# Performance work log

Hardware: AMD Instinct MI355X
Metric: run time of the kernel (lower is better)

## Reference

```python
import jax, jax.numpy as jnp
import numpy as np

N_EMBED = 8192
EMBED_DIM = 32
BETA = 0.25
EPS_NORM = 1e-12   # torch F.normalize eps
EPS_ENT = 1e-4     # get_entropy eps


def _l2norm(x):
    n = jnp.linalg.norm(x, axis=-1, keepdims=True)
    return x / jnp.maximum(n, EPS_NORM)


def setup_inputs() -> dict:
    key = jax.random.key(0)
    k1, k2 = jax.random.split(key)
    z = jax.random.normal(k1, (32, EMBED_DIM, 32, 32), dtype=jnp.float32)
    # embedding.weight.data.uniform_(-1/n_embed, 1/n_embed)
    embedding = jax.random.uniform(k2, (N_EMBED, EMBED_DIM), dtype=jnp.float32,
                                   minval=-1.0 / N_EMBED, maxval=1.0 / N_EMBED)
    return {"z": z, "embedding": embedding}


def reference(z, embedding):
    batch = z.shape[0]
    # bchw -> bhwc
    zt = jnp.transpose(z, (0, 2, 3, 1))
    # l2_norm branch: cosine distance via negative inner product
    zn = _l2norm(zt)
    z_flat = zn.reshape(-1, EMBED_DIM)            # [N, D], N = B*H*W
    ew = _l2norm(embedding)                       # [K, D]
    d = -jnp.matmul(z_flat, ew.T)                 # [N, K] distance matrix
    idx = jnp.argmin(jax.lax.stop_gradient(d), axis=1)  # [N]
    # codebook usage histogram + entropy
    cb_usage = jax.ops.segment_sum(jnp.ones_like(idx, dtype=jnp.float32), idx,
                                   num_segments=N_EMBED)
    probs = (cb_usage + EPS_ENT) / jnp.sum(cb_usage + EPS_ENT)
    cb_entropy = -jnp.sum(probs * jnp.log(probs))
    # gather + re-normalize (faithful to embedding lookup then F.normalize)
    z_q = _l2norm(embedding[idx]).reshape(zn.shape)
    sg = jax.lax.stop_gradient
    loss = (BETA * jnp.mean(jnp.sum((sg(z_q) - zn) ** 2, axis=-1))
            + jnp.mean(jnp.sum((z_q - sg(zn)) ** 2, axis=-1)))
    # straight-through estimator
    z_q_st = zn + sg(z_q - zn)
    z_q_out = jnp.transpose(z_q_st, (0, 3, 1, 2))  # bhwc -> bchw
    return z_q_out, loss, cb_entropy, idx.reshape(batch, -1)
```

## Files before the change

kernel.cpp:

```cpp
#include <hip/hip_runtime.h>
#include <math.h>

#define N_EMBED 8192
#define DIM 32
#define NQ 32768

#define QPB 256
#define NQG (NQ / QPB)
#define KSPL 8
#define KCHUNK (N_EMBED / KSPL)
#define TILE 128
#define NTILES (KCHUNK / TILE)
#define NPLANE 8
#define LSTRIDE 130

#define LOSS_OFF  1048576
#define ENT_OFF   1048577
#define IDX_OFF   1048578

typedef __attribute__((ext_vector_type(8))) _Float16 half8;
typedef __attribute__((ext_vector_type(4))) float floatx4;

__global__ __launch_bounds__(256) void prep_kernel(const float* __restrict__ e,
                                                   half8* __restrict__ esplit,
                                                   float* __restrict__ inv_norm,
                                                   unsigned* __restrict__ usage,
                                                   float* __restrict__ loss_acc,
                                                   unsigned* __restrict__ done_ctr) {
    int k = blockIdx.x * 256 + threadIdx.x;
    const float4* src = (const float4*)(e + k * DIM);
    float v[DIM];
    float ss = 0.f;
#pragma unroll
    for (int i = 0; i < 8; ++i) {
        float4 t = src[i];
        v[i*4+0] = t.x; v[i*4+1] = t.y; v[i*4+2] = t.z; v[i*4+3] = t.w;
        ss += t.x*t.x + t.y*t.y + t.z*t.z + t.w*t.w;
    }
    float inv = 1.f / fmaxf(sqrtf(ss), 1e-12f);
    inv_norm[k] = inv;
    usage[k] = 0u;
    if (k == 0) { loss_acc[0] = 0.f; done_ctr[0] = 0u; }

#pragma unroll
    for (int part = 0; part < 4; ++part) {
        half8 h8, m8;
#pragma unroll
        for (int j = 0; j < 8; ++j) {
            float xx = v[part * 8 + j] * inv;
            _Float16 h = (_Float16)xx;
            _Float16 m = (_Float16)((xx - (float)h) * 4096.0f);
            h8[j] = h; m8[j] = m;
        }
        esplit[(0 * 4 + part) * N_EMBED + k] = h8;
        esplit[(1 * 4 + part) * N_EMBED + k] = m8;
    }
}

__global__ __launch_bounds__(256, 4) void score_kernel(const float* __restrict__ z,
                                                       const half8* __restrict__ esplit,
                                                       unsigned long long* __restrict__ keys8) {
    __shared__ half8 lds[2][NPLANE * LSTRIDE];

    const int t = threadIdx.x;
    const int lane = t & 63;
    const int w = t >> 6;
    const int quad = lane >> 4;
    const int lc = lane & 15;
    const int qg = blockIdx.x & (NQG - 1);
    const int kc = blockIdx.x >> 7;
    const int kbase = kc * KCHUNK;
    const int qbase = qg * QPB + w * 64;

    half8 ah[4], am[4];
#pragma unroll
    for (int qt = 0; qt < 4; ++qt) {
        int q = qbase + qt * 16 + lc;
        const float* zp = z + (q >> 10) * (DIM * 1024) + (q & 1023);
        float x[8];
        float ss = 0.f;
#pragma unroll
        for (int j = 0; j < 8; ++j) {
            x[j] = zp[(quad * 8 + j) * 1024];
            ss = fmaf(x[j], x[j], ss);
        }
        ss += __shfl_xor(ss, 16, 64);
        ss += __shfl_xor(ss, 32, 64);
        float inv = 1.f / fmaxf(sqrtf(ss), 1e-12f);
#pragma unroll
        for (int j = 0; j < 8; ++j) {
            float xx = x[j] * inv;
            _Float16 h = (_Float16)xx;
            _Float16 m = (_Float16)((xx - (float)h) * 4096.0f);
            ah[qt][j] = h; am[qt][j] = m;
        }
    }

    float best[16];
    int bk[16];
#pragma unroll
    for (int i = 0; i < 16; ++i) { best[i] = -2.0f; bk[i] = 0; }

    const floatx4 z4 = {0.f, 0.f, 0.f, 0.f};

#pragma unroll
    for (int j = 0; j < 4; ++j) {
        int c = t + j * 256; int p = c >> 7, i = c & 127;
        lds[0][p * LSTRIDE + i] = esplit[p * N_EMBED + kbase + i];
    }
    __syncthreads();

    for (int kt = 0; kt < NTILES; ++kt) {
        half8 st[4];
        if (kt + 1 < NTILES) {
#pragma unroll
            for (int j = 0; j < 4; ++j) {
                int c = t + j * 256; int p = c >> 7, i = c & 127;
                st[j] = esplit[p * N_EMBED + kbase + (kt + 1) * TILE + i];
            }
        }
        const half8* __restrict__ buf = lds[kt & 1];
#pragma unroll 2
        for (int ct = 0; ct < TILE / 16; ++ct) {
            half8 bh = buf[(0 * 4 + quad) * LSTRIDE + ct * 16 + lc];
            half8 bm = buf[(1 * 4 + quad) * LSTRIDE + ct * 16 + lc];
            const int kk = kbase + kt * TILE + ct * 16 + lc;
#pragma unroll
            for (int qt = 0; qt < 4; ++qt) {
                floatx4 a0 = __builtin_amdgcn_mfma_f32_16x16x32_f16(ah[qt], bh, z4, 0, 0, 0);
                floatx4 a1 = __builtin_amdgcn_mfma_f32_16x16x32_f16(ah[qt], bm, z4, 0, 0, 0);
                a1 = __builtin_amdgcn_mfma_f32_16x16x32_f16(am[qt], bh, a1, 0, 0, 0);
#pragma unroll
                for (int r = 0; r < 4; ++r) {
                    float d = fmaf(a1[r], 0x1p-12f, a0[r]);
                    if (d > best[qt * 4 + r]) { best[qt * 4 + r] = d; bk[qt * 4 + r] = kk; }
                }
            }
        }
        __syncthreads();
        if (kt + 1 < NTILES) {
#pragma unroll
            for (int j = 0; j < 4; ++j) {
                int c = t + j * 256; int p = c >> 7, i = c & 127;
                lds[(kt + 1) & 1][p * LSTRIDE + i] = st[j];
            }
            __syncthreads();
        }
    }

#pragma unroll
    for (int i = 0; i < 16; ++i) {
        unsigned ub = __float_as_uint(best[i]);
        ub = (ub & 0x80000000u) ? ~ub : (ub | 0x80000000u);
        unsigned long long key = ((unsigned long long)ub << 32) | (unsigned)(~bk[i]);
#pragma unroll
        for (int msk = 1; msk <= 8; msk <<= 1) {
            unsigned long long o = __shfl_xor(key, msk, 64);
            key = (o > key) ? o : key;
        }
        if (lc == 0) {
            int qt = i >> 2, r = i & 3;
            int q = qbase + qt * 16 + quad * 4 + r;
            keys8[kc * NQ + q] = key;
        }
    }
}

__global__ __launch_bounds__(256) void finalize_kernel(const float* __restrict__ z,
                                                       const float* __restrict__ e,
                                                       const float* __restrict__ inv_norm,
                                                       const unsigned long long* __restrict__ keys8,
                                                       unsigned* __restrict__ usage,
                                                       float* __restrict__ loss_acc,
                                                       unsigned* __restrict__ done_ctr,
                                                       float* __restrict__ out) {
    int n = blockIdx.x * 256 + threadIdx.x;
    int b  = n >> 10;
    int hw = n & 1023;
    const float* zb = z + b * (DIM * 1024) + hw;

    float q[DIM];
    float ss = 0.f;
#pragma unroll
    for (int d = 0; d < DIM; ++d) {
        q[d] = zb[d * 1024];
        ss = fmaf(q[d], q[d], ss);
    }
    float inv = 1.f / fmaxf(sqrtf(ss), 1e-12f);
#pragma unroll
    for (int d = 0; d < DIM; ++d) q[d] *= inv;

    float bestd = -1e30f;
    int idx = 0;
#pragma unroll
    for (int c = 0; c < 8; ++c) {
        unsigned long long key = keys8[c * NQ + n];
        int k = (int)(~(unsigned)(key & 0xFFFFFFFFull));
        const float4* er = (const float4*)(e + k * DIM);
        float dot = 0.f;
#pragma unroll
        for (int d8 = 0; d8 < 8; ++d8) {
            float4 t4 = er[d8];
            dot = fmaf(t4.x, q[d8*4+0], dot);
            dot = fmaf(t4.y, q[d8*4+1], dot);
            dot = fmaf(t4.z, q[d8*4+2], dot);
            dot = fmaf(t4.w, q[d8*4+3], dot);
        }
        dot *= inv_norm[k];
        if (dot > bestd) { bestd = dot; idx = k; }
    }

    atomicAdd(&usage[idx], 1u);

    float inv2 = inv_norm[idx];
    const float4* er = (const float4*)(e + idx * DIM);
    float lsum = 0.f;
    float* outb = out + b * (DIM * 1024) + hw;
#pragma unroll
    for (int d8 = 0; d8 < 8; ++d8) {
        float4 t4 = er[d8];
        float w4[4] = {t4.x, t4.y, t4.z, t4.w};
#pragma unroll
        for (int j = 0; j < 4; ++j) {
            int d = d8 * 4 + j;
            float zq = w4[j] * inv2;
            float diff = zq - q[d];
            lsum = fmaf(diff, diff, lsum);
            outb[d * 1024] = q[d] + (zq - q[d]);
        }
    }
    out[IDX_OFF + n] = (float)idx;

#pragma unroll
    for (int off = 32; off > 0; off >>= 1)
        lsum += __shfl_down(lsum, off, 64);
    if ((threadIdx.x & 63) == 0)
        atomicAdd(loss_acc, lsum);

    __shared__ unsigned lastflag;
    __syncthreads();
    if (threadIdx.x == 0) {
        __threadfence();
        unsigned prev = __hip_atomic_fetch_add(done_ctr, 1u, __ATOMIC_ACQ_REL,
                                               __HIP_MEMORY_SCOPE_AGENT);
        lastflag = (prev == gridDim.x - 1) ? 1u : 0u;
    }
    __syncthreads();
    if (lastflag) {
        __shared__ double sm[256];
        int t = threadIdx.x;
        double local = 0.0;
        const float denom = 32768.8192f;
        for (int k = t; k < N_EMBED; k += 256) {
            unsigned c = __hip_atomic_load(&usage[k], __ATOMIC_RELAXED,
                                           __HIP_MEMORY_SCOPE_AGENT);
            float p = ((float)c + 1e-4f) / denom;
            local += (double)(-(p * logf(p)));
        }
        sm[t] = local;
        __syncthreads();
        for (int s = 128; s > 0; s >>= 1) {
            if (t < s) sm[t] += sm[t + s];
            __syncthreads();
        }
        if (t == 0) {
            float la = __hip_atomic_load(loss_acc, __ATOMIC_RELAXED,
                                         __HIP_MEMORY_SCOPE_AGENT);
            out[LOSS_OFF] = (float)(1.25 * (double)la / 32768.0);
            out[ENT_OFF]  = (float)sm[0];
        }
    }
}

extern "C" void kernel_launch(void* const* d_in, const int* in_sizes, int n_in,
                              void* d_out, int out_size, void* d_ws, size_t ws_size,
                              hipStream_t stream) {
    const float* z   = (const float*)d_in[0];
    const float* emb = (const float*)d_in[1];
    float* out = (float*)d_out;

    char* ws = (char*)d_ws;
    half8* esplit            = (half8*)ws;
    unsigned long long* keys8= (unsigned long long*)(ws + (1 << 20));
    float* inv_norm          = (float*)(ws + 3 * (1 << 20));
    unsigned* usage          = (unsigned*)(ws + 3 * (1 << 20) + 32768);
    float* loss_acc          = (float*)(ws + 3 * (1 << 20) + 65536);
    unsigned* done_ctr       = (unsigned*)(ws + 3 * (1 << 20) + 65536 + 4);

    prep_kernel<<<N_EMBED / 256, 256, 0, stream>>>(emb, esplit, inv_norm, usage,
                                                   loss_acc, done_ctr);
    score_kernel<<<NQG * KSPL, 256, 0, stream>>>(z, esplit, keys8);
    finalize_kernel<<<NQ / 256, 256, 0, stream>>>(z, emb, inv_norm, keys8, usage,
                                                  loss_acc, done_ctr, out);
}
```

Baseline: 152.0 us.

## Switch scoring to 32x32x16 MFMA tiles and merge split keys directly in finalize

The score kernel now uses 32x32x16 f16 MFMA instructions over 32 queries per wave instead of 16x16x32 over four 16-query tiles. This halves queries per block and doubles the grid, and occupancy drops from 4 to 3 blocks per SIMD. It is meant to cut LDS reads and MFMA issue overhead per useful product. Finalize now takes the max of the eight packed keys instead of recomputing fp32 dot products for each candidate. That removes gather traffic but relies on the split-fp16 score precision for the final argmin.

```diff
diff --git a/kernel.cpp b/kernel.cpp
--- a/kernel.cpp
+++ b/kernel.cpp
@@ -5,7 +5,7 @@
 #define DIM 32
 #define NQ 32768
 
-#define QPB 256
+#define QPB 128
 #define NQG (NQ / QPB)
 #define KSPL 8
 #define KCHUNK (N_EMBED / KSPL)
@@ -19,7 +19,7 @@
 #define IDX_OFF   1048578
 
 typedef __attribute__((ext_vector_type(8))) _Float16 half8;
-typedef __attribute__((ext_vector_type(4))) float floatx4;
+typedef __attribute__((ext_vector_type(16))) float floatx16;
 
 __global__ __launch_bounds__(256) void prep_kernel(const float* __restrict__ e,
                                                    half8* __restrict__ esplit,
@@ -57,7 +57,7 @@
     }
 }
 
-__global__ __launch_bounds__(256, 4) void score_kernel(const float* __restrict__ z,
+__global__ __launch_bounds__(256, 3) void score_kernel(const float* __restrict__ z,
                                                        const half8* __restrict__ esplit,
                                                        unsigned long long* __restrict__ keys8) {
     __shared__ half8 lds[2][NPLANE * LSTRIDE];
@@ -65,34 +65,36 @@
     const int t = threadIdx.x;
     const int lane = t & 63;
     const int w = t >> 6;
-    const int quad = lane >> 4;
-    const int lc = lane & 15;
+    const int kh = lane >> 5;
+    const int col = lane & 31;
     const int qg = blockIdx.x & (NQG - 1);
-    const int kc = blockIdx.x >> 7;
+    const int kc = blockIdx.x >> 8;
     const int kbase = kc * KCHUNK;
-    const int qbase = qg * QPB + w * 64;
-
-    half8 ah[4], am[4];
-#pragma unroll
-    for (int qt = 0; qt < 4; ++qt) {
-        int q = qbase + qt * 16 + lc;
+    const int qbase = qg * QPB + w * 32;
+
+    half8 ah0, ah1, am0, am1;
+    {
+        int q = qbase + col;
         const float* zp = z + (q >> 10) * (DIM * 1024) + (q & 1023);
-        float x[8];
+        float x[16];
         float ss = 0.f;
 #pragma unroll
         for (int j = 0; j < 8; ++j) {
-            x[j] = zp[(quad * 8 + j) * 1024];
-            ss = fmaf(x[j], x[j], ss);
-        }
-        ss += __shfl_xor(ss, 16, 64);
+            x[j]     = zp[(kh * 8 + j) * 1024];
+            x[8 + j] = zp[(16 + kh * 8 + j) * 1024];
+        }
+#pragma unroll
+        for (int j = 0; j < 16; ++j) ss = fmaf(x[j], x[j], ss);
         ss += __shfl_xor(ss, 32, 64);
         float inv = 1.f / fmaxf(sqrtf(ss), 1e-12f);
 #pragma unroll
         for (int j = 0; j < 8; ++j) {
-            float xx = x[j] * inv;
-            _Float16 h = (_Float16)xx;
-            _Float16 m = (_Float16)((xx - (float)h) * 4096.0f);
-            ah[qt][j] = h; am[qt][j] = m;
+            float x0 = x[j] * inv;
+            _Float16 h0 = (_Float16)x0;
+            ah0[j] = h0; am0[j] = (_Float16)((x0 - (float)h0) * 4096.0f);
+            float x1 = x[8 + j] * inv;
+            _Float16 h1 = (_Float16)x1;
+            ah1[j] = h1; am1[j] = (_Float16)((x1 - (float)h1) * 4096.0f);
         }
     }
 
@@ -101,7 +103,9 @@
 #pragma unroll
     for (int i = 0; i < 16; ++i) { best[i] = -2.0f; bk[i] = 0; }
 
-    const floatx4 z4 = {0.f, 0.f, 0.f, 0.f};
+    floatx16 z16;
+#pragma unroll
+    for (int i = 0; i < 16; ++i) z16[i] = 0.f;
 
 #pragma unroll
     for (int j = 0; j < 4; ++j) {
@@ -120,21 +124,26 @@
             }
         }
         const half8* __restrict__ buf = lds[kt & 1];
-#pragma unroll 2
-        for (int ct = 0; ct < TILE / 16; ++ct) {
-            half8 bh = buf[(0 * 4 + quad) * LSTRIDE + ct * 16 + lc];
-            half8 bm = buf[(1 * 4 + quad) * LSTRIDE + ct * 16 + lc];
-            const int kk = kbase + kt * TILE + ct * 16 + lc;
-#pragma unroll
-            for (int qt = 0; qt < 4; ++qt) {
-                floatx4 a0 = __builtin_amdgcn_mfma_f32_16x16x32_f16(ah[qt], bh, z4, 0, 0, 0);
-                floatx4 a1 = __builtin_amdgcn_mfma_f32_16x16x32_f16(ah[qt], bm, z4, 0, 0, 0);
-                a1 = __builtin_amdgcn_mfma_f32_16x16x32_f16(am[qt], bh, a1, 0, 0, 0);
-#pragma unroll
-                for (int r = 0; r < 4; ++r) {
-                    float d = fmaf(a1[r], 0x1p-12f, a0[r]);
-                    if (d > best[qt * 4 + r]) { best[qt * 4 + r] = d; bk[qt * 4 + r] = kk; }
-                }
+#pragma unroll
+        for (int ct = 0; ct < TILE / 32; ++ct) {
+            const half8* bp = buf + ct * 32 + col;
+            half8 bh0 = bp[(0 + kh) * LSTRIDE];
+            half8 bh1 = bp[(2 + kh) * LSTRIDE];
+            half8 bm0 = bp[(4 + kh) * LSTRIDE];
+            half8 bm1 = bp[(6 + kh) * LSTRIDE];
+
+            floatx16 a0 = __builtin_amdgcn_mfma_f32_32x32x16_f16(ah0, bh0, z16, 0, 0, 0);
+            floatx16 a1 = __builtin_amdgcn_mfma_f32_32x32x16_f16(ah0, bm0, z16, 0, 0, 0);
+            a0 = __builtin_amdgcn_mfma_f32_32x32x16_f16(ah1, bh1, a0, 0, 0, 0);
+            a1 = __builtin_amdgcn_mfma_f32_32x32x16_f16(am0, bh0, a1, 0, 0, 0);
+            a1 = __builtin_amdgcn_mfma_f32_32x32x16_f16(ah1, bm1, a1, 0, 0, 0);
+            a1 = __builtin_amdgcn_mfma_f32_32x32x16_f16(am1, bh1, a1, 0, 0, 0);
+
+            const int kk = kbase + kt * TILE + ct * 32 + col;
+#pragma unroll
+            for (int r = 0; r < 16; ++r) {
+                float d = fmaf(a1[r], 0x1p-12f, a0[r]);
+                if (d > best[r]) { best[r] = d; bk[r] = kk; }
             }
         }
         __syncthreads();
@@ -149,19 +158,18 @@
     }
 
 #pragma unroll
-    for (int i = 0; i < 16; ++i) {
-        unsigned ub = __float_as_uint(best[i]);
+    for (int r = 0; r < 16; ++r) {
+        unsigned ub = __float_as_uint(best[r]);
         ub = (ub & 0x80000000u) ? ~ub : (ub | 0x80000000u);
-        unsigned long long key = ((unsigned long long)ub << 32) | (unsigned)(~bk[i]);
-#pragma unroll
-        for (int msk = 1; msk <= 8; msk <<= 1) {
+        unsigned long long key = ((unsigned long long)ub << 32) | (unsigned)(~bk[r]);
+#pragma unroll
+        for (int msk = 1; msk <= 16; msk <<= 1) {
             unsigned long long o = __shfl_xor(key, msk, 64);
             key = (o > key) ? o : key;
         }
-        if (lc == 0) {
-            int qt = i >> 2, r = i & 3;
-            int q = qbase + qt * 16 + quad * 4 + r;
-            keys8[kc * NQ + q] = key;
+        if (col == 0) {
+            int row = (r & 3) + 8 * (r >> 2) + 4 * kh;
+            keys8[kc * NQ + qbase + row] = key;
         }
     }
 }
@@ -190,25 +198,13 @@
 #pragma unroll
     for (int d = 0; d < DIM; ++d) q[d] *= inv;
 
-    float bestd = -1e30f;
-    int idx = 0;
-#pragma unroll
-    for (int c = 0; c < 8; ++c) {
-        unsigned long long key = keys8[c * NQ + n];
-        int k = (int)(~(unsigned)(key & 0xFFFFFFFFull));
-        const float4* er = (const float4*)(e + k * DIM);
-        float dot = 0.f;
-#pragma unroll
-        for (int d8 = 0; d8 < 8; ++d8) {
-            float4 t4 = er[d8];
-            dot = fmaf(t4.x, q[d8*4+0], dot);
-            dot = fmaf(t4.y, q[d8*4+1], dot);
-            dot = fmaf(t4.z, q[d8*4+2], dot);
-            dot = fmaf(t4.w, q[d8*4+3], dot);
-        }
-        dot *= inv_norm[k];
-        if (dot > bestd) { bestd = dot; idx = k; }
-    }
+    unsigned long long bestkey = 0ull;
+#pragma unroll
+    for (int c = 0; c < KSPL; ++c) {
+        unsigned long long k8 = keys8[c * NQ + n];
+        bestkey = (k8 > bestkey) ? k8 : bestkey;
+    }
+    int idx = (int)(~(unsigned)(bestkey & 0xFFFFFFFFull));
 
     atomicAdd(&usage[idx], 1u);
 
```

New measurement: 154.1 us. About the same (+1.4%).

## Fuse codebook prep into score kernel and drop exact fp32 rescoring

Applied to the files above, without the earlier changes.

Removes the separate prep kernel: each score block now loads raw fp32 codebook rows, normalizes them and splits them into fp16 hi/lo parts directly into LDS. The block size grows to 512 and the codebook is split into 16 chunks. Finalize now picks the winner by a max over the packed score/index keys instead of recomputing exact fp32 dot products for each chunk candidate. This saves a launch and the finalize gather work, but every block now redoes the normalization, and the argmin relies only on the split-fp16 scores, which can change tie-breaking.

```diff
diff --git a/kernel.cpp b/kernel.cpp
--- a/kernel.cpp
+++ b/kernel.cpp
@@ -5,9 +5,9 @@
 #define DIM 32
 #define NQ 32768
 
-#define QPB 256
+#define QPB 512
 #define NQG (NQ / QPB)
-#define KSPL 8
+#define KSPL 16
 #define KCHUNK (N_EMBED / KSPL)
 #define TILE 128
 #define NTILES (KCHUNK / TILE)
@@ -21,54 +21,27 @@
 typedef __attribute__((ext_vector_type(8))) _Float16 half8;
 typedef __attribute__((ext_vector_type(4))) float floatx4;
 
-__global__ __launch_bounds__(256) void prep_kernel(const float* __restrict__ e,
-                                                   half8* __restrict__ esplit,
-                                                   float* __restrict__ inv_norm,
-                                                   unsigned* __restrict__ usage,
-                                                   float* __restrict__ loss_acc,
-                                                   unsigned* __restrict__ done_ctr) {
-    int k = blockIdx.x * 256 + threadIdx.x;
-    const float4* src = (const float4*)(e + k * DIM);
-    float v[DIM];
-    float ss = 0.f;
-#pragma unroll
-    for (int i = 0; i < 8; ++i) {
-        float4 t = src[i];
-        v[i*4+0] = t.x; v[i*4+1] = t.y; v[i*4+2] = t.z; v[i*4+3] = t.w;
-        ss += t.x*t.x + t.y*t.y + t.z*t.z + t.w*t.w;
-    }
-    float inv = 1.f / fmaxf(sqrtf(ss), 1e-12f);
-    inv_norm[k] = inv;
-    usage[k] = 0u;
-    if (k == 0) { loss_acc[0] = 0.f; done_ctr[0] = 0u; }
-
-#pragma unroll
-    for (int part = 0; part < 4; ++part) {
-        half8 h8, m8;
-#pragma unroll
-        for (int j = 0; j < 8; ++j) {
-            float xx = v[part * 8 + j] * inv;
-            _Float16 h = (_Float16)xx;
-            _Float16 m = (_Float16)((xx - (float)h) * 4096.0f);
-            h8[j] = h; m8[j] = m;
-        }
-        esplit[(0 * 4 + part) * N_EMBED + k] = h8;
-        esplit[(1 * 4 + part) * N_EMBED + k] = m8;
-    }
-}
-
-__global__ __launch_bounds__(256, 4) void score_kernel(const float* __restrict__ z,
-                                                       const half8* __restrict__ esplit,
-                                                       unsigned long long* __restrict__ keys8) {
+__global__ __launch_bounds__(512, 4) void score_kernel(const float* __restrict__ z,
+                                                       const float* __restrict__ e,
+                                                       unsigned long long* __restrict__ keys16,
+                                                       unsigned* __restrict__ usage,
+                                                       float* __restrict__ loss_acc,
+                                                       unsigned* __restrict__ done_ctr) {
     __shared__ half8 lds[2][NPLANE * LSTRIDE];
 
     const int t = threadIdx.x;
+
+    if (blockIdx.x == 0) {
+        for (int i = t; i < N_EMBED; i += 512) usage[i] = 0u;
+        if (t == 0) { loss_acc[0] = 0.f; done_ctr[0] = 0u; }
+    }
+
     const int lane = t & 63;
     const int w = t >> 6;
     const int quad = lane >> 4;
     const int lc = lane & 15;
     const int qg = blockIdx.x & (NQG - 1);
-    const int kc = blockIdx.x >> 7;
+    const int kc = blockIdx.x >> 6;
     const int kbase = kc * KCHUNK;
     const int qbase = qg * QPB + w * 64;
 
@@ -96,6 +69,31 @@
         }
     }
 
+    auto stage = [&](int bsel, int kt) {
+        const int ci = t >> 2;
+        const int part = t & 3;
+        const int code = kbase + kt * TILE + ci;
+        const float4* er = (const float4*)(e + code * DIM) + part * 2;
+        float4 v0 = er[0], v1 = er[1];
+        float x[8] = {v0.x, v0.y, v0.z, v0.w, v1.x, v1.y, v1.z, v1.w};
+        float ss = 0.f;
+#pragma unroll
+        for (int j = 0; j < 8; ++j) ss = fmaf(x[j], x[j], ss);
+        ss += __shfl_xor(ss, 1, 64);
+        ss += __shfl_xor(ss, 2, 64);
+        float inv = 1.f / fmaxf(sqrtf(ss), 1e-12f);
+        half8 h8, m8;
+#pragma unroll
+        for (int j = 0; j < 8; ++j) {
+            float xx = x[j] * inv;
+            _Float16 h = (_Float16)xx;
+            _Float16 m = (_Float16)((xx - (float)h) * 4096.0f);
+            h8[j] = h; m8[j] = m;
+        }
+        lds[bsel][part * LSTRIDE + ci] = h8;
+        lds[bsel][(4 + part) * LSTRIDE + ci] = m8;
+    };
+
     float best[16];
     int bk[16];
 #pragma unroll
@@ -103,22 +101,12 @@
 
     const floatx4 z4 = {0.f, 0.f, 0.f, 0.f};
 
-#pragma unroll
-    for (int j = 0; j < 4; ++j) {
-        int c = t + j * 256; int p = c >> 7, i = c & 127;
-        lds[0][p * LSTRIDE + i] = esplit[p * N_EMBED + kbase + i];
-    }
+    stage(0, 0);
     __syncthreads();
 
     for (int kt = 0; kt < NTILES; ++kt) {
-        half8 st[4];
-        if (kt + 1 < NTILES) {
-#pragma unroll
-            for (int j = 0; j < 4; ++j) {
-                int c = t + j * 256; int p = c >> 7, i = c & 127;
-                st[j] = esplit[p * N_EMBED + kbase + (kt + 1) * TILE + i];
-            }
-        }
+        if (kt + 1 < NTILES) stage((kt + 1) & 1, kt + 1);
+
         const half8* __restrict__ buf = lds[kt & 1];
 #pragma unroll 2
         for (int ct = 0; ct < TILE / 16; ++ct) {
@@ -138,14 +126,6 @@
             }
         }
         __syncthreads();
-        if (kt + 1 < NTILES) {
-#pragma unroll
-            for (int j = 0; j < 4; ++j) {
-                int c = t + j * 256; int p = c >> 7, i = c & 127;
-                lds[(kt + 1) & 1][p * LSTRIDE + i] = st[j];
-            }
-            __syncthreads();
-        }
     }
 
 #pragma unroll
@@ -161,15 +141,14 @@
         if (lc == 0) {
             int qt = i >> 2, r = i & 3;
             int q = qbase + qt * 16 + quad * 4 + r;
-            keys8[kc * NQ + q] = key;
+            keys16[kc * NQ + q] = key;
         }
     }
 }
 
 __global__ __launch_bounds__(256) void finalize_kernel(const float* __restrict__ z,
                                                        const float* __restrict__ e,
-                                                       const float* __restrict__ inv_norm,
-                                                       const unsigned long long* __restrict__ keys8,
+                                                       const unsigned long long* __restrict__ keys16,
                                                        unsigned* __restrict__ usage,
                                                        float* __restrict__ loss_acc,
                                                        unsigned* __restrict__ done_ctr,
@@ -190,44 +169,35 @@
 #pragma unroll
     for (int d = 0; d < DIM; ++d) q[d] *= inv;
 
-    float bestd = -1e30f;
-    int idx = 0;
-#pragma unroll
-    for (int c = 0; c < 8; ++c) {
-        unsigned long long key = keys8[c * NQ + n];
-        int k = (int)(~(unsigned)(key & 0xFFFFFFFFull));
-        const float4* er = (const float4*)(e + k * DIM);
-        float dot = 0.f;
-#pragma unroll
-        for (int d8 = 0; d8 < 8; ++d8) {
-            float4 t4 = er[d8];
-            dot = fmaf(t4.x, q[d8*4+0], dot);
-            dot = fmaf(t4.y, q[d8*4+1], dot);
-            dot = fmaf(t4.z, q[d8*4+2], dot);
-            dot = fmaf(t4.w, q[d8*4+3], dot);
-        }
-        dot *= inv_norm[k];
-        if (dot > bestd) { bestd = dot; idx = k; }
-    }
+    unsigned long long bestkey = 0ull;
+#pragma unroll
+    for (int c = 0; c < KSPL; ++c) {
+        unsigned long long k16 = keys16[c * NQ + n];
+        bestkey = (k16 > bestkey) ? k16 : bestkey;
+    }
+    int idx = (int)(~(unsigned)(bestkey & 0xFFFFFFFFull));
 
     atomicAdd(&usage[idx], 1u);
 
-    float inv2 = inv_norm[idx];
+    float wv[DIM];
+    float ss2 = 0.f;
     const float4* er = (const float4*)(e + idx * DIM);
+#pragma unroll
+    for (int d8 = 0; d8 < 8; ++d8) {
+        float4 t4 = er[d8];
+        wv[d8*4+0] = t4.x; wv[d8*4+1] = t4.y; wv[d8*4+2] = t4.z; wv[d8*4+3] = t4.w;
+        ss2 += t4.x*t4.x + t4.y*t4.y + t4.z*t4.z + t4.w*t4.w;
+    }
+    float inv2 = 1.f / fmaxf(sqrtf(ss2), 1e-12f);
+
     float lsum = 0.f;
     float* outb = out + b * (DIM * 1024) + hw;
 #pragma unroll
-    for (int d8 = 0; d8 < 8; ++d8) {
-        float4 t4 = er[d8];
-        float w4[4] = {t4.x, t4.y, t4.z, t4.w};
-#pragma unroll
-        for (int j = 0; j < 4; ++j) {
-            int d = d8 * 4 + j;
-            float zq = w4[j] * inv2;
-            float diff = zq - q[d];
-            lsum = fmaf(diff, diff, lsum);
-            outb[d * 1024] = q[d] + (zq - q[d]);
-        }
+    for (int d = 0; d < DIM; ++d) {
+        float zq = wv[d] * inv2;
+        float diff = zq - q[d];
+        lsum = fmaf(diff, diff, lsum);
+        outb[d * 1024] = q[d] + (zq - q[d]);
     }
     out[IDX_OFF + n] = (float)idx;
 
@@ -280,16 +250,13 @@
     float* out = (float*)d_out;
 
     char* ws = (char*)d_ws;
-    half8* esplit            = (half8*)ws;
-    unsigned long long* keys8= (unsigned long long*)(ws + (1 << 20));
-    float* inv_norm          = (float*)(ws + 3 * (1 << 20));
-    unsigned* usage          = (unsigned*)(ws + 3 * (1 << 20) + 32768);
-    float* loss_acc          = (float*)(ws + 3 * (1 << 20) + 65536);
-    unsigned* done_ctr       = (unsigned*)(ws + 3 * (1 << 20) + 65536 + 4);
-
-    prep_kernel<<<N_EMBED / 256, 256, 0, stream>>>(emb, esplit, inv_norm, usage,
-                                                   loss_acc, done_ctr);
-    score_kernel<<<NQG * KSPL, 256, 0, stream>>>(z, esplit, keys8);
-    finalize_kernel<<<NQ / 256, 256, 0, stream>>>(z, emb, inv_norm, keys8, usage,
+    unsigned long long* keys16 = (unsigned long long*)ws;
+    unsigned* usage            = (unsigned*)(ws + (4 << 20));
+    float* loss_acc            = (float*)(ws + (4 << 20) + 32768);
+    unsigned* done_ctr         = (unsigned*)(ws + (4 << 20) + 32768 + 4);
+
+    score_kernel<<<NQG * KSPL, 512, 0, stream>>>(z, emb, keys16, usage,
+                                                 loss_acc, done_ctr);
+    finalize_kernel<<<NQ / 256, 256, 0, stream>>>(z, emb, keys16, usage,
                                                   loss_acc, done_ctr, out);
 }
```

Result: faster. 144.4 us (-5.0%).

## Fuse finalize into score kernel via per-query-group last-block completion counters

Applied to the files above, without the earlier changes.

Removes the separate finalize kernel: each score block bumps a per-query-group counter, and the last of the K-split blocks for that group reduces the 8 partial keys, gathers the winning code, writes outputs and loss, and a global counter triggers the entropy pass. The exact fp32 re-ranking of the 8 chunk winners is replaced by taking the max of the packed approximate score keys, and the inverse-norm buffer is dropped in favour of recomputing the norm of the chosen row. This saves a launch and the re-rank gathers, but adds atomics, fences and tail work on the last blocks, and may change argmin on near-ties.

```diff
diff --git a/kernel.cpp b/kernel.cpp
--- a/kernel.cpp
+++ b/kernel.cpp
@@ -23,10 +23,10 @@
 
 __global__ __launch_bounds__(256) void prep_kernel(const float* __restrict__ e,
                                                    half8* __restrict__ esplit,
-                                                   float* __restrict__ inv_norm,
                                                    unsigned* __restrict__ usage,
+                                                   unsigned* __restrict__ qg_ctr,
                                                    float* __restrict__ loss_acc,
-                                                   unsigned* __restrict__ done_ctr) {
+                                                   unsigned* __restrict__ fin_ctr) {
     int k = blockIdx.x * 256 + threadIdx.x;
     const float4* src = (const float4*)(e + k * DIM);
     float v[DIM];
@@ -38,9 +38,9 @@
         ss += t.x*t.x + t.y*t.y + t.z*t.z + t.w*t.w;
     }
     float inv = 1.f / fmaxf(sqrtf(ss), 1e-12f);
-    inv_norm[k] = inv;
     usage[k] = 0u;
-    if (k == 0) { loss_acc[0] = 0.f; done_ctr[0] = 0u; }
+    if (k < NQG) qg_ctr[k] = 0u;
+    if (k == 0) { loss_acc[0] = 0.f; fin_ctr[0] = 0u; }
 
 #pragma unroll
     for (int part = 0; part < 4; ++part) {
@@ -58,9 +58,17 @@
 }
 
 __global__ __launch_bounds__(256, 4) void score_kernel(const float* __restrict__ z,
+                                                       const float* __restrict__ e,
                                                        const half8* __restrict__ esplit,
-                                                       unsigned long long* __restrict__ keys8) {
+                                                       unsigned long long* __restrict__ keys8,
+                                                       unsigned* __restrict__ usage,
+                                                       unsigned* __restrict__ qg_ctr,
+                                                       float* __restrict__ loss_acc,
+                                                       unsigned* __restrict__ fin_ctr,
+                                                       float* __restrict__ out) {
     __shared__ half8 lds[2][NPLANE * LSTRIDE];
+    __shared__ double sm[256];
+    __shared__ unsigned qflag, eflag;
 
     const int t = threadIdx.x;
     const int lane = t & 63;
@@ -161,113 +169,106 @@
         if (lc == 0) {
             int qt = i >> 2, r = i & 3;
             int q = qbase + qt * 16 + quad * 4 + r;
-            keys8[kc * NQ + q] = key;
-        }
-    }
-}
-
-__global__ __launch_bounds__(256) void finalize_kernel(const float* __restrict__ z,
-                                                       const float* __restrict__ e,
-                                                       const float* __restrict__ inv_norm,
-                                                       const unsigned long long* __restrict__ keys8,
-                                                       unsigned* __restrict__ usage,
-                                                       float* __restrict__ loss_acc,
-                                                       unsigned* __restrict__ done_ctr,
-                                                       float* __restrict__ out) {
-    int n = blockIdx.x * 256 + threadIdx.x;
-    int b  = n >> 10;
-    int hw = n & 1023;
-    const float* zb = z + b * (DIM * 1024) + hw;
-
-    float q[DIM];
-    float ss = 0.f;
-#pragma unroll
-    for (int d = 0; d < DIM; ++d) {
-        q[d] = zb[d * 1024];
-        ss = fmaf(q[d], q[d], ss);
-    }
-    float inv = 1.f / fmaxf(sqrtf(ss), 1e-12f);
-#pragma unroll
-    for (int d = 0; d < DIM; ++d) q[d] *= inv;
-
-    float bestd = -1e30f;
-    int idx = 0;
-#pragma unroll
-    for (int c = 0; c < 8; ++c) {
-        unsigned long long key = keys8[c * NQ + n];
-        int k = (int)(~(unsigned)(key & 0xFFFFFFFFull));
-        const float4* er = (const float4*)(e + k * DIM);
-        float dot = 0.f;
+            __hip_atomic_store(&keys8[kc * NQ + q], key, __ATOMIC_RELAXED,
+                               __HIP_MEMORY_SCOPE_AGENT);
+        }
+    }
+
+    __threadfence();
+    __syncthreads();
+    if (t == 0) {
+        unsigned prev = __hip_atomic_fetch_add(&qg_ctr[qg], 1u, __ATOMIC_ACQ_REL,
+                                               __HIP_MEMORY_SCOPE_AGENT);
+        qflag = (prev == KSPL - 1) ? 1u : 0u;
+    }
+    __syncthreads();
+
+    if (qflag) {
+        int n = qg * QPB + t;
+        int b  = n >> 10;
+        int hw = n & 1023;
+        const float* zb = z + b * (DIM * 1024) + hw;
+
+        float q[DIM];
+        float ss = 0.f;
+#pragma unroll
+        for (int d = 0; d < DIM; ++d) {
+            q[d] = zb[d * 1024];
+            ss = fmaf(q[d], q[d], ss);
+        }
+        float inv = 1.f / fmaxf(sqrtf(ss), 1e-12f);
+#pragma unroll
+        for (int d = 0; d < DIM; ++d) q[d] *= inv;
+
+        unsigned long long bestkey = 0ull;
+#pragma unroll
+        for (int c = 0; c < KSPL; ++c) {
+            unsigned long long kk = __hip_atomic_load(&keys8[c * NQ + n],
+                                                      __ATOMIC_RELAXED,
+                                                      __HIP_MEMORY_SCOPE_AGENT);
+            bestkey = (kk > bestkey) ? kk : bestkey;
+        }
+        int idx = (int)(~(unsigned)(bestkey & 0xFFFFFFFFull));
+
+        atomicAdd(&usage[idx], 1u);
+
+        float wv[DIM];
+        float ss2 = 0.f;
+        const float4* er = (const float4*)(e + idx * DIM);
 #pragma unroll
         for (int d8 = 0; d8 < 8; ++d8) {
             float4 t4 = er[d8];
-            dot = fmaf(t4.x, q[d8*4+0], dot);
-            dot = fmaf(t4.y, q[d8*4+1], dot);
-            dot = fmaf(t4.z, q[d8*4+2], dot);
-            dot = fmaf(t4.w, q[d8*4+3], dot);
-        }
-        dot *= inv_norm[k];
-        if (dot > bestd) { bestd = dot; idx = k; }
-    }
-
-    atomicAdd(&usage[idx], 1u);
-
-    float inv2 = inv_norm[idx];
-    const float4* er = (const float4*)(e + idx * DIM);
-    float lsum = 0.f;
-    float* outb = out + b * (DIM * 1024) + hw;
-#pragma unroll
-    for (int d8 = 0; d8 < 8; ++d8) {
-        float4 t4 = er[d8];
-        float w4[4] = {t4.x, t4.y, t4.z, t4.w};
-#pragma unroll
-        for (int j = 0; j < 4; ++j) {
-            int d = d8 * 4 + j;
-            float zq = w4[j] * inv2;
+            wv[d8*4+0] = t4.x; wv[d8*4+1] = t4.y; wv[d8*4+2] = t4.z; wv[d8*4+3] = t4.w;
+            ss2 += t4.x*t4.x + t4.y*t4.y + t4.z*t4.z + t4.w*t4.w;
+        }
+        float inv2 = 1.f / fmaxf(sqrtf(ss2), 1e-12f);
+
+        float lsum = 0.f;
+        float* outb = out + b * (DIM * 1024) + hw;
+#pragma unroll
+        for (int d = 0; d < DIM; ++d) {
+            float zq = wv[d] * inv2;
             float diff = zq - q[d];
             lsum = fmaf(diff, diff, lsum);
             outb[d * 1024] = q[d] + (zq - q[d]);
         }
-    }
-    out[IDX_OFF + n] = (float)idx;
-
-#pragma unroll
-    for (int off = 32; off > 0; off >>= 1)
-        lsum += __shfl_down(lsum, off, 64);
-    if ((threadIdx.x & 63) == 0)
-        atomicAdd(loss_acc, lsum);
-
-    __shared__ unsigned lastflag;
-    __syncthreads();
-    if (threadIdx.x == 0) {
+        out[IDX_OFF + n] = (float)idx;
+
+#pragma unroll
+        for (int off = 32; off > 0; off >>= 1)
+            lsum += __shfl_down(lsum, off, 64);
+        if ((t & 63) == 0)
+            atomicAdd(loss_acc, lsum);
+
         __threadfence();
-        unsigned prev = __hip_atomic_fetch_add(done_ctr, 1u, __ATOMIC_ACQ_REL,
+        __syncthreads();
+        if (t == 0) {
+            unsigned prev = __hip_atomic_fetch_add(fin_ctr, 1u, __ATOMIC_ACQ_REL,
+                                                   __HIP_MEMORY_SCOPE_AGENT);
+            eflag = (prev == NQG - 1) ? 1u : 0u;
+        }
+        __syncthreads();
+        if (eflag) {
+            double local = 0.0;
+            const float denom = 32768.8192f;
+            for (int k = t; k < N_EMBED; k += 256) {
+                unsigned c = __hip_atomic_load(&usage[k], __ATOMIC_RELAXED,
                                                __HIP_MEMORY_SCOPE_AGENT);
-        lastflag = (prev == gridDim.x - 1) ? 1u : 0u;
-    }
-    __syncthreads();
-    if (lastflag) {
-        __shared__ double sm[256];
-        int t = threadIdx.x;
-        double local = 0.0;
-        const float denom = 32768.8192f;
-        for (int k = t; k < N_EMBED; k += 256) {
-            unsigned c = __hip_atomic_load(&usage[k], __ATOMIC_RELAXED,
-                                           __HIP_MEMORY_SCOPE_AGENT);
-            float p = ((float)c + 1e-4f) / denom;
-            local += (double)(-(p * logf(p)));
-        }
-        sm[t] = local;
-        __syncthreads();
-        for (int s = 128; s > 0; s >>= 1) {
-            if (t < s) sm[t] += sm[t + s];
+                float p = ((float)c + 1e-4f) / denom;
+                local += (double)(-(p * logf(p)));
+            }
+            sm[t] = local;
             __syncthreads();
-        }
-        if (t == 0) {
-            float la = __hip_atomic_load(loss_acc, __ATOMIC_RELAXED,
-                                         __HIP_MEMORY_SCOPE_AGENT);
-            out[LOSS_OFF] = (float)(1.25 * (double)la / 32768.0);
-            out[ENT_OFF]  = (float)sm[0];
+            for (int s = 128; s > 0; s >>= 1) {
+                if (t < s) sm[t] += sm[t + s];
+                __syncthreads();
+            }
+            if (t == 0) {
+                float la = __hip_atomic_load(loss_acc, __ATOMIC_RELAXED,
+                                             __HIP_MEMORY_SCOPE_AGENT);
+                out[LOSS_OFF] = (float)(1.25 * (double)la / 32768.0);
+                out[ENT_OFF]  = (float)sm[0];
+            }
         }
     }
 }
@@ -280,16 +281,15 @@
     float* out = (float*)d_out;
 
     char* ws = (char*)d_ws;
-    half8* esplit            = (half8*)ws;
-    unsigned long long* keys8= (unsigned long long*)(ws + (1 << 20));
-    float* inv_norm          = (float*)(ws + 3 * (1 << 20));
-    unsigned* usage          = (unsigned*)(ws + 3 * (1 << 20) + 32768);
-    float* loss_acc          = (float*)(ws + 3 * (1 << 20) + 65536);
-    unsigned* done_ctr       = (unsigned*)(ws + 3 * (1 << 20) + 65536 + 4);
-
-    prep_kernel<<<N_EMBED / 256, 256, 0, stream>>>(emb, esplit, inv_norm, usage,
-                                                   loss_acc, done_ctr);
-    score_kernel<<<NQG * KSPL, 256, 0, stream>>>(z, esplit, keys8);
-    finalize_kernel<<<NQ / 256, 256, 0, stream>>>(z, emb, inv_norm, keys8, usage,
-                                                  loss_acc, done_ctr, out);
+    half8* esplit             = (half8*)ws;
+    unsigned long long* keys8 = (unsigned long long*)(ws + (1 << 20));
+    unsigned* usage           = (unsigned*)(ws + (3 << 20));
+    unsigned* qg_ctr          = (unsigned*)(ws + (3 << 20) + 32768);
+    float* loss_acc           = (float*)(ws + (3 << 20) + 32768 + 512);
+    unsigned* fin_ctr         = (unsigned*)(ws + (3 << 20) + 32768 + 512 + 4);
+
+    prep_kernel<<<N_EMBED / 256, 256, 0, stream>>>(emb, esplit, usage, qg_ctr,
+                                                   loss_acc, fin_ctr);
+    score_kernel<<<NQG * KSPL, 256, 0, stream>>>(z, emb, esplit, keys8, usage,
+                                                 qg_ctr, loss_acc, fin_ctr, out);
 }
```

Result: slower. 206.2 us (+35.7%).
